# Performance work log

Measured on AMD Instinct MI355X. Metric: run time of the kernel, lower is better.

The kernel has to match this reference:

```python
import jax, jax.numpy as jnp
import numpy as np

H = 8          # attention heads
EPS = 1e-5     # LayerNorm eps (torch default)
B, T, E = 8, 1024, 128
D, DI, N, DC, R = 512, 1024, 16, 4, 32   # d_model, d_inner, d_state, d_conv, dt_rank
NT, NM = 6, 8                            # transformer layers, mamba layers
FF = 2048                                # transformer dim_feedforward (torch default)


def setup_inputs():
    key = jax.random.key(0)
    ks = iter(jax.random.split(key, 48))
    def rn(shape, scale=0.05):
        return jax.random.normal(next(ks), shape, jnp.float32) * scale
    return {
        "emb":      jax.random.normal(next(ks), (B, T, E), jnp.float32),
        # TransformerEncoder (6 post-norm layers), params stacked on leading layer dim
        "t_wqkv":   rn((NT, 3 * E, E)), "t_bqkv": jnp.zeros((NT, 3 * E), jnp.float32),
        "t_wo":     rn((NT, E, E)),     "t_bo":   jnp.zeros((NT, E), jnp.float32),
        "t_ln1w":   jnp.ones((NT, E), jnp.float32),  "t_ln1b": jnp.zeros((NT, E), jnp.float32),
        "t_w1":     rn((NT, FF, E)),    "t_b1":   jnp.zeros((NT, FF), jnp.float32),
        "t_w2":     rn((NT, E, FF)),    "t_b2":   jnp.zeros((NT, E), jnp.float32),
        "t_ln2w":   jnp.ones((NT, E), jnp.float32),  "t_ln2b": jnp.zeros((NT, E), jnp.float32),
        # Linear(emb_dim -> d_model)
        "w_in":     rn((D, E)), "b_in": jnp.zeros((D,), jnp.float32),
        # MambaBlocks (8 raw Mamba layers, no residual/norm), stacked
        "m_inproj": rn((NM, 2 * DI, D)),
        "m_convw":  rn((NM, DI, DC), 0.2), "m_convb": jnp.zeros((NM, DI), jnp.float32),
        "m_xproj":  rn((NM, R + 2 * N, DI)),
        "m_dtw":    rn((NM, DI, R), 0.1),
        "m_dtb":    jax.random.uniform(next(ks), (NM, DI), jnp.float32, -6.0, -3.0),
        "m_Alog":   jnp.log(jnp.tile(jnp.arange(1, N + 1, dtype=jnp.float32), (NM, DI, 1))),
        "m_D":      jnp.ones((NM, DI), jnp.float32),
        "m_outproj": rn((NM, D, DI)),
        # Linear(d_model -> emb_dim)
        "w_out":    rn((E, D)), "b_out": jnp.zeros((E,), jnp.float32),
    }


def _ln(x, w, b):
    mu = jnp.mean(x, -1, keepdims=True)
    var = jnp.var(x, -1, keepdims=True)
    return (x - mu) * jax.lax.rsqrt(var + EPS) * w + b


def _tlayer(x, p):
    wqkv, bqkv, wo, bo, ln1w, ln1b, w1, b1, w2, b2, ln2w, ln2b = p
    qkv = x @ wqkv.T + bqkv                        # (B,T,3E)
    q, k, v = jnp.split(qkv, 3, axis=-1)
    def heads(t):                                  # (B,T,E) -> (B,H,T,E//H)
        return t.reshape(B, T, H, E // H).transpose(0, 2, 1, 3)
    q, k, v = heads(q), heads(k), heads(v)
    scores = jnp.einsum("bhqd,bhkd->bhqk", q, k) / jnp.sqrt(jnp.float32(E // H))
    attn = jax.nn.softmax(scores, axis=-1)
    o = jnp.einsum("bhqk,bhkd->bhqd", attn, v).transpose(0, 2, 1, 3).reshape(B, T, E)
    x = _ln(x + o @ wo.T + bo, ln1w, ln1b)         # post-norm (torch default)
    ff = jax.nn.relu(x @ w1.T + b1) @ w2.T + b2
    return _ln(x + ff, ln2w, ln2b)


def _mamba_layer(x, p):
    inproj, convw, convb, xproj, dtw, dtb, Alog, Dp, outproj = p
    xz = x @ inproj.T                              # (B,T,2*DI)
    xi, z = jnp.split(xz, 2, axis=-1)
    # causal depthwise conv1d, kernel DC, left-padded
    xp = jnp.pad(xi, ((0, 0), (DC - 1, 0), (0, 0)))
    conv = sum(xp[:, k:k + T, :] * convw[:, k] for k in range(DC)) + convb
    xi = jax.nn.silu(conv)
    dbc = xi @ xproj.T                             # (B,T,R+2N)
    dt_r, Bt, Ct = dbc[..., :R], dbc[..., R:R + N], dbc[..., R + N:]
    dt = jax.nn.softplus(dt_r @ dtw.T + dtb)       # (B,T,DI)
    A = -jnp.exp(Alog)                             # (DI,N)
    def step(h, inputs):
        dt_t, B_t, C_t, x_t = inputs               # (B,DI),(B,N),(B,N),(B,DI)
        dA = jnp.exp(dt_t[:, :, None] * A)         # (B,DI,N)
        h = h * dA + (dt_t * x_t)[:, :, None] * B_t[:, None, :]
        y = jnp.einsum("bdn,bn->bd", h, C_t)
        return h, y
    h0 = jnp.zeros((B, DI, N), x.dtype)
    seq = (dt.transpose(1, 0, 2), Bt.transpose(1, 0, 2),
           Ct.transpose(1, 0, 2), xi.transpose(1, 0, 2))
    _, ys = jax.lax.scan(step, h0, seq)            # ys: (T,B,DI)
    y = ys.transpose(1, 0, 2) + Dp * xi
    y = y * jax.nn.silu(z)
    return y @ outproj.T                           # (B,T,D)


def reference(emb, t_wqkv, t_bqkv, t_wo, t_bo, t_ln1w, t_ln1b, t_w1, t_b1, t_w2, t_b2,
              t_ln2w, t_ln2b, w_in, b_in, m_inproj, m_convw, m_convb, m_xproj, m_dtw,
              m_dtb, m_Alog, m_D, m_outproj, w_out, b_out):
    x = emb
    tparams = (t_wqkv, t_bqkv, t_wo, t_bo, t_ln1w, t_ln1b, t_w1, t_b1, t_w2, t_b2, t_ln2w, t_ln2b)
    for i in range(NT):
        x = _tlayer(x, tuple(p[i] for p in tparams))
    x = x @ w_in.T + b_in                          # (B,T,D)
    mparams = (m_inproj, m_convw, m_convb, m_xproj, m_dtw, m_dtb, m_Alog, m_D, m_outproj)
    for i in range(NM):
        x = _mamba_layer(x, tuple(p[i] for p in mparams))
    return x @ w_out.T + b_out                     # (B,T,E)
```

## Files before the change

kernel.cpp:

```cpp
#include <hip/hip_runtime.h>
#include <math.h>

#define HB 8
#define TT 1024
#define NSTATE 16
#define NTT 6
#define NMM 8
#define MM (HB*TT)
#define EPSV 1e-5f
#define CHUNK 64
#define NCH (TT/CHUNK)
#define LSTR 72
#define AKS 128
#define VSTR 132

typedef _Float16 f16x8 __attribute__((ext_vector_type(8)));
typedef _Float16 f16x4 __attribute__((ext_vector_type(4)));
typedef float f32x4_t __attribute__((ext_vector_type(4)));

static __device__ inline void split8(const float4 a, const float4 b,
                                     f16x8& h, f16x8& l)
{
  float x[8] = {a.x, a.y, a.z, a.w, b.x, b.y, b.z, b.w};
#pragma unroll
  for (int i = 0; i < 8; i++) {
    _Float16 hi = (_Float16)x[i];
    h[i] = hi;
    l[i] = (_Float16)(x[i] - (float)hi);
  }
}

__global__ __launch_bounds__(256) void split_k(
    const float* __restrict__ X, _Float16* __restrict__ Hi,
    _Float16* __restrict__ Lo)
{
  const size_t i = ((size_t)blockIdx.x * 256 + threadIdx.x) * 4;
  float4 v = *(const float4*)&X[i];
  float x[4] = {v.x, v.y, v.z, v.w};
  f16x4 h, l;
#pragma unroll
  for (int j = 0; j < 4; j++) {
    _Float16 hi = (_Float16)x[j];
    h[j] = hi;
    l[j] = (_Float16)(x[j] - (float)hi);
  }
  *(f16x4*)&Hi[i] = h;
  *(f16x4*)&Lo[i] = l;
}

template<int TN>
__global__ __launch_bounds__(256) void gemm_mfma_t(
    const float* __restrict__ A, int lda,
    const float* __restrict__ W,
    const _Float16* __restrict__ Ahi, const _Float16* __restrict__ Alo,
    const _Float16* __restrict__ Whi, const _Float16* __restrict__ Wlo,
    const float* __restrict__ bias,
    float* __restrict__ C,
    float* __restrict__ P,
    int N, int K, int S, int act)
{
  __shared__ _Float16 As[128 * LSTR];
  __shared__ _Float16 Bs[TN * LSTR];
  const int tid = threadIdx.x;
  const int m0 = blockIdx.y * 128;
  const int n0 = blockIdx.x * TN;
  const int z = blockIdx.z;
  const int kchunk = K / S;
  const int kb = z * kchunk;
  const int ke = kb + kchunk;

  const int lr = tid >> 1;
  const int lh = tid & 1;
  const int lane = tid & 63;
  const int w = tid >> 6;
  const int quad = lane >> 4;
  const int l16 = lane & 15;

  const float* Arow = A + (size_t)(m0 + lr) * lda + lh * 16;
  const _Float16* AHrow = Ahi ? (Ahi + (size_t)(m0 + lr) * lda + lh * 16) : nullptr;
  const _Float16* ALrow = Ahi ? (Alo + (size_t)(m0 + lr) * lda + lh * 16) : nullptr;
  _Float16* Adst = &As[lr * LSTR + lh * 16];

  constexpr int MI = (TN == 128) ? 4 : 2;
  const int w0 = (TN == 128) ? (w & 1) : w;
  const int w1 = (TN == 128) ? (w >> 1) : 0;
  const int rowbase = (TN == 128) ? w0 * 64 : w0 * 32;

  f32x4_t acc[MI][4];
#pragma unroll
  for (int i = 0; i < MI; i++)
#pragma unroll
    for (int j = 0; j < 4; j++)
#pragma unroll
      for (int r = 0; r < 4; r++) acc[i][j][r] = 0.f;

  const _Float16* ab = &As[(rowbase + l16) * LSTR + quad * 8];
  const _Float16* bb = &Bs[(w1 * 64 + l16) * LSTR + quad * 8];

  const float* Wrow;
  const _Float16* WHrow = nullptr;
  const _Float16* WLrow = nullptr;
  _Float16* Bdst;
  if (TN == 128) {
    Wrow = W + (size_t)(n0 + lr) * K + lh * 16;
    if (Whi) {
      WHrow = Whi + (size_t)(n0 + lr) * K + lh * 16;
      WLrow = Wlo + (size_t)(n0 + lr) * K + lh * 16;
    }
    Bdst = &Bs[lr * LSTR + lh * 16];
  } else {
    const int br = tid >> 2;
    const int bo = (tid & 3) * 8;
    Wrow = W + (size_t)(n0 + br) * K + bo;
    if (Whi) {
      WHrow = Whi + (size_t)(n0 + br) * K + bo;
      WLrow = Wlo + (size_t)(n0 + br) * K + bo;
    }
    Bdst = &Bs[br * LSTR + bo];
  }

  for (int k0 = kb; k0 < ke; k0 += 32) {
    f16x8 ah0, ah1, al0, al1;
    float4 a0, a1, a2, a3;
    if (Ahi) {
      ah0 = *(const f16x8*)&AHrow[k0];
      ah1 = *(const f16x8*)&AHrow[k0 + 8];
      al0 = *(const f16x8*)&ALrow[k0];
      al1 = *(const f16x8*)&ALrow[k0 + 8];
    } else {
      a0 = *(const float4*)&Arow[k0];
      a1 = *(const float4*)&Arow[k0 + 4];
      a2 = *(const float4*)&Arow[k0 + 8];
      a3 = *(const float4*)&Arow[k0 + 12];
    }
    f16x8 wh0, wh1, wl0, wl1;
    float4 b0, b1, b2, b3;
    if (Whi) {
      wh0 = *(const f16x8*)&WHrow[k0];
      wl0 = *(const f16x8*)&WLrow[k0];
      if (TN == 128) {
        wh1 = *(const f16x8*)&WHrow[k0 + 8];
        wl1 = *(const f16x8*)&WLrow[k0 + 8];
      }
    } else {
      b0 = *(const float4*)&Wrow[k0];
      b1 = *(const float4*)&Wrow[k0 + 4];
      if (TN == 128) {
        b2 = *(const float4*)&Wrow[k0 + 8];
        b3 = *(const float4*)&Wrow[k0 + 12];
      }
    }
    __syncthreads();
    if (Ahi) {
      *(f16x8*)&Adst[0] = ah0; *(f16x8*)&Adst[8] = ah1;
      *(f16x8*)&Adst[32] = al0; *(f16x8*)&Adst[40] = al1;
    } else {
      f16x8 h, l;
      split8(a0, a1, h, l);
      *(f16x8*)&Adst[0] = h; *(f16x8*)&Adst[32] = l;
      split8(a2, a3, h, l);
      *(f16x8*)&Adst[8] = h; *(f16x8*)&Adst[40] = l;
    }
    if (Whi) {
      *(f16x8*)&Bdst[0] = wh0; *(f16x8*)&Bdst[32] = wl0;
      if (TN == 128) { *(f16x8*)&Bdst[8] = wh1; *(f16x8*)&Bdst[40] = wl1; }
    } else {
      f16x8 h, l;
      split8(b0, b1, h, l);
      *(f16x8*)&Bdst[0] = h; *(f16x8*)&Bdst[32] = l;
      if (TN == 128) {
        split8(b2, b3, h, l);
        *(f16x8*)&Bdst[8] = h; *(f16x8*)&Bdst[40] = l;
      }
    }
    __syncthreads();

    f16x8 bh[4], bl[4];
#pragma unroll
    for (int ni = 0; ni < 4; ni++) {
      bh[ni] = *(const f16x8*)&bb[ni * 16 * LSTR];
      bl[ni] = *(const f16x8*)&bb[ni * 16 * LSTR + 32];
    }
#pragma unroll
    for (int mi = 0; mi < MI; mi++) {
      f16x8 fah = *(const f16x8*)&ab[mi * 16 * LSTR];
      f16x8 fal = *(const f16x8*)&ab[mi * 16 * LSTR + 32];
#pragma unroll
      for (int ni = 0; ni < 4; ni++) {
        acc[mi][ni] = __builtin_amdgcn_mfma_f32_16x16x32_f16(fah, bh[ni], acc[mi][ni], 0, 0, 0);
        acc[mi][ni] = __builtin_amdgcn_mfma_f32_16x16x32_f16(fah, bl[ni], acc[mi][ni], 0, 0, 0);
        acc[mi][ni] = __builtin_amdgcn_mfma_f32_16x16x32_f16(fal, bh[ni], acc[mi][ni], 0, 0, 0);
      }
    }
  }

  float* dst = (S == 1) ? C : (P + (size_t)z * MM * N);
#pragma unroll
  for (int ni = 0; ni < 4; ni++) {
    const int n = n0 + w1 * 64 + ni * 16 + l16;
    const float bv = (S == 1 && bias) ? bias[n] : 0.f;
#pragma unroll
    for (int mi = 0; mi < MI; mi++) {
      const int mbase = m0 + rowbase + mi * 16 + quad * 4;
#pragma unroll
      for (int r = 0; r < 4; r++) {
        float v = acc[mi][ni][r] + bv;
        if (S == 1) {
          if (act == 1) v = fmaxf(v, 0.f);
          else if (act == 2) v = fmaxf(v, 0.f) + log1pf(__expf(-fabsf(v)));
        }
        dst[(size_t)(mbase + r) * N + n] = v;
      }
    }
  }
}

__global__ __launch_bounds__(256) void reduce_k(
    const float* __restrict__ P, const float* __restrict__ bias,
    float* __restrict__ C, int nmask, int S, int act, int stride4)
{
  const int idx = blockIdx.x * 256 + threadIdx.x;
  float4 a = *(const float4*)&P[(size_t)idx * 4];
  for (int z = 1; z < S; z++) {
    float4 p = *(const float4*)&P[(size_t)(idx + z * (size_t)stride4) * 4];
    a.x += p.x; a.y += p.y; a.z += p.z; a.w += p.w;
  }
  if (bias) {
    float4 bv = *(const float4*)&bias[(idx * 4) & nmask];
    a.x += bv.x; a.y += bv.y; a.z += bv.z; a.w += bv.w;
  }
  if (act == 1) {
    a.x = fmaxf(a.x, 0.f); a.y = fmaxf(a.y, 0.f);
    a.z = fmaxf(a.z, 0.f); a.w = fmaxf(a.w, 0.f);
  } else if (act == 2) {
    a.x = fmaxf(a.x, 0.f) + log1pf(__expf(-fabsf(a.x)));
    a.y = fmaxf(a.y, 0.f) + log1pf(__expf(-fabsf(a.y)));
    a.z = fmaxf(a.z, 0.f) + log1pf(__expf(-fabsf(a.z)));
    a.w = fmaxf(a.w, 0.f) + log1pf(__expf(-fabsf(a.w)));
  }
  *(float4*)&C[(size_t)idx * 4] = a;
}

__global__ __launch_bounds__(256) void attn_mfma_k(
    const float* __restrict__ qkv, float* __restrict__ o)
{
  __shared__ _Float16 Khi[AKS * 16], Klo[AKS * 16];
  __shared__ _Float16 Vthi[16 * VSTR], Vtlo[16 * VSTR];
  __shared__ float Pscr[4][16 * 18];

  const int tid = threadIdx.x;
  const int lane = tid & 63;
  const int wv = tid >> 6;
  const int quad = lane >> 4;
  const int l16 = lane & 15;
  const int qh = quad & 1;
  const int bh = blockIdx.y;
  const int b = bh >> 3;
  const int h = bh & 7;
  const int qb0 = blockIdx.x * 128;

  f16x8 qa[2];
#pragma unroll
  for (int u = 0; u < 2; u++) {
    const int qrow = qb0 + wv * 32 + u * 16 + l16;
    const float* qp = qkv + (size_t)(b * TT + qrow) * 384 + h * 16 + qh * 8;
    float4 x0 = *(const float4*)&qp[0];
    float4 x1 = *(const float4*)&qp[4];
    float xv[8] = {x0.x, x0.y, x0.z, x0.w, x1.x, x1.y, x1.z, x1.w};
#pragma unroll
    for (int j = 0; j < 8; j++) {
      float q = xv[j] * 0.25f;
      _Float16 hi = (_Float16)q;
      _Float16 lo = (_Float16)(q - (float)hi);
      qa[u][j] = (quad < 2) ? hi : lo;
    }
  }

  f32x4_t oacc[2];
  float lacc[2][4];
#pragma unroll
  for (int u = 0; u < 2; u++)
#pragma unroll
    for (int r = 0; r < 4; r++) { oacc[u][r] = 0.f; lacc[u][r] = 0.f; }

  float* Pw = &Pscr[wv][0];

  for (int ks = 0; ks < TT; ks += AKS) {
    __syncthreads();
    {
      const int key = tid >> 1, hf = tid & 1;
      const float* kp = qkv + (size_t)(b * TT + ks + key) * 384 + 128 + h * 16 + hf * 8;
      float4 k0 = *(const float4*)&kp[0];
      float4 k1 = *(const float4*)&kp[4];
      f16x8 vh, vl;
      split8(k0, k1, vh, vl);
      *(f16x8*)&Khi[key * 16 + hf * 8] = vh;
      *(f16x8*)&Klo[key * 16 + hf * 8] = vl;
      const float* vp = kp + 128;
      float4 v0 = *(const float4*)&vp[0];
      float4 v1 = *(const float4*)&vp[4];
      float vvv[8] = {v0.x, v0.y, v0.z, v0.w, v1.x, v1.y, v1.z, v1.w};
#pragma unroll
      for (int j = 0; j < 8; j++) {
        const int d = hf * 8 + j;
        _Float16 hi = (_Float16)vvv[j];
        Vthi[d * VSTR + key] = hi;
        Vtlo[d * VSTR + key] = (_Float16)(vvv[j] - (float)hi);
      }
    }
    __syncthreads();

    for (int kt = 0; kt < AKS; kt += 16) {
      f16x8 kfh = *(const f16x8*)&Khi[(kt + l16) * 16 + qh * 8];
      f16x8 kfl = *(const f16x8*)&Klo[(kt + l16) * 16 + qh * 8];
      const int vo = l16 * VSTR + kt + qh * 8;
      f16x4 va0 = *(const f16x4*)&Vthi[vo];
      f16x4 va1 = *(const f16x4*)&Vthi[vo + 4];
      f16x4 vb0 = *(const f16x4*)&Vtlo[vo];
      f16x4 vb1 = *(const f16x4*)&Vtlo[vo + 4];
      f16x8 vfh, vfl;
#pragma unroll
      for (int i = 0; i < 4; i++) {
        vfh[i] = va0[i]; vfh[4 + i] = va1[i];
        vfl[i] = vb0[i]; vfl[4 + i] = vb1[i];
      }

#pragma unroll
      for (int u = 0; u < 2; u++) {
        f32x4_t s;
#pragma unroll
        for (int r = 0; r < 4; r++) s[r] = 0.f;
        s = __builtin_amdgcn_mfma_f32_16x16x32_f16(qa[u], kfh, s, 0, 0, 0);
        s = __builtin_amdgcn_mfma_f32_16x16x32_f16(qa[u], kfl, s, 0, 0, 0);
        float p[4];
#pragma unroll
        for (int r = 0; r < 4; r++) {
          p[r] = __expf(s[r]);
          lacc[u][r] += p[r];
        }
        float* ps = Pw + (quad * 4) * 18 + l16;
        ps[0] = p[0]; ps[18] = p[1]; ps[36] = p[2]; ps[54] = p[3];
        __asm__ volatile("s_waitcnt lgkmcnt(0)" ::: "memory");
        const float* pr = Pw + l16 * 18 + qh * 8;
        f16x8 pa;
#pragma unroll
        for (int j = 0; j < 8; j++) {
          float pv = pr[j];
          _Float16 hi = (_Float16)pv;
          _Float16 lo = (_Float16)(pv - (float)hi);
          pa[j] = (quad < 2) ? hi : lo;
        }
        oacc[u] = __builtin_amdgcn_mfma_f32_16x16x32_f16(pa, vfh, oacc[u], 0, 0, 0);
        oacc[u] = __builtin_amdgcn_mfma_f32_16x16x32_f16(pa, vfl, oacc[u], 0, 0, 0);
        __asm__ volatile("s_waitcnt lgkmcnt(0)" ::: "memory");
      }
    }
  }

#pragma unroll
  for (int u = 0; u < 2; u++) {
#pragma unroll
    for (int r = 0; r < 4; r++) {
      float lv = lacc[u][r];
      lv += __shfl_xor(lv, 1);
      lv += __shfl_xor(lv, 2);
      lv += __shfl_xor(lv, 4);
      lv += __shfl_xor(lv, 8);
      const float inv = 1.f / lv;
      const int qrow = qb0 + wv * 32 + u * 16 + quad * 4 + r;
      o[(size_t)(b * TT + qrow) * 128 + h * 16 + l16] = oacc[u][r] * inv;
    }
  }
}

__global__ __launch_bounds__(256) void add_ln_k(
    const float* __restrict__ a, const float* __restrict__ bvec,
    const float* __restrict__ w, const float* __restrict__ bb,
    float* __restrict__ out)
{
  const int tid = threadIdx.x;
  const int wave = tid >> 6, lane = tid & 63;
  const size_t row = (size_t)blockIdx.x * 4 + wave;
  const float* pa = a + row * 128;
  const float* pb = bvec + row * 128;
  float v0 = pa[lane] + pb[lane];
  float v1 = pa[lane + 64] + pb[lane + 64];
  float s1 = v0 + v1, s2 = v0 * v0 + v1 * v1;
#pragma unroll
  for (int off = 32; off; off >>= 1) {
    s1 += __shfl_down(s1, off);
    s2 += __shfl_down(s2, off);
  }
  s1 = __shfl(s1, 0); s2 = __shfl(s2, 0);
  const float mean = s1 * (1.f / 128.f);
  const float var = s2 * (1.f / 128.f) - mean * mean;
  const float rs = rsqrtf(var + EPSV);
  out[row * 128 + lane]      = (v0 - mean) * rs * w[lane] + bb[lane];
  out[row * 128 + lane + 64] = (v1 - mean) * rs * w[lane + 64] + bb[lane + 64];
}

__global__ __launch_bounds__(256) void conv_silu_k(
    const float* __restrict__ xz, const float* __restrict__ cw,
    const float* __restrict__ cb, float* __restrict__ out)
{
  const int idx = blockIdx.x * 256 + threadIdx.x;
  const int di = idx & 1023;
  const int m = idx >> 10;
  const int t = m & (TT - 1);
  float acc = cb[di];
#pragma unroll
  for (int k = 0; k < 4; k++) {
    int tt = t + k - 3;
    if (tt >= 0) acc += xz[(size_t)(m + k - 3) * 2048 + di] * cw[di * 4 + k];
  }
  out[(size_t)m * 1024 + di] = acc / (1.f + __expf(-acc));
}

__global__ __launch_bounds__(64) void scan_partial_k(
    const float* __restrict__ dt,
    const float* __restrict__ dbc,
    const float* __restrict__ xi,
    const float* __restrict__ Alog,
    float* __restrict__ Pb, float* __restrict__ Sb)
{
  const int slice = blockIdx.x & 15;
  const int c = blockIdx.x >> 4;
  const int b = blockIdx.y;
  const int di = slice * 64 + threadIdx.x;

  float A[NSTATE];
#pragma unroll
  for (int n = 0; n < NSTATE; n++) A[n] = -__expf(Alog[di * NSTATE + n]);
  float h[NSTATE], P[NSTATE];
#pragma unroll
  for (int n = 0; n < NSTATE; n++) { h[n] = 0.f; P[n] = 1.f; }

  const size_t m0 = (size_t)b * TT + (size_t)c * CHUNK;
  for (int t = 0; t < CHUNK; t++) {
    const size_t m = m0 + t;
    const float dtv = dt[m * 1024 + di];
    const float xv  = xi[m * 1024 + di];
    const float dtx = dtv * xv;
#pragma unroll
    for (int n = 0; n < NSTATE; n++) {
      const float Bv = dbc[m * 64 + 32 + n];
      const float dA = __expf(dtv * A[n]);
      h[n] = h[n] * dA + dtx * Bv;
      P[n] *= dA;
    }
  }
  const size_t base = (((size_t)b * NCH + c) * NSTATE) * 1024 + di;
#pragma unroll
  for (int n = 0; n < NSTATE; n++) {
    Pb[base + (size_t)n * 1024] = P[n];
    Sb[base + (size_t)n * 1024] = h[n];
  }
}

__global__ __launch_bounds__(256) void scan_fix_k(
    float* __restrict__ Pb, const float* __restrict__ Sb)
{
  const int idx = blockIdx.x * 256 + threadIdx.x;
  const int b = idx >> 10;
  const int di = idx & 1023;
  float h[NSTATE];
#pragma unroll
  for (int n = 0; n < NSTATE; n++) h[n] = 0.f;
  for (int c = 0; c < NCH; c++) {
    const size_t base = (((size_t)b * NCH + c) * NSTATE) * 1024 + di;
    float P[NSTATE], S[NSTATE];
#pragma unroll
    for (int n = 0; n < NSTATE; n++) {
      P[n] = Pb[base + (size_t)n * 1024];
      S[n] = Sb[base + (size_t)n * 1024];
    }
#pragma unroll
    for (int n = 0; n < NSTATE; n++) {
      Pb[base + (size_t)n * 1024] = h[n];
      h[n] = P[n] * h[n] + S[n];
    }
  }
}

__global__ __launch_bounds__(64) void scan_final_k(
    const float* __restrict__ dt,
    const float* __restrict__ dbc,
    const float* __restrict__ xi,
    const float* __restrict__ xz,
    const float* __restrict__ Alog,
    const float* __restrict__ Dp,
    const float* __restrict__ Hin,
    float* __restrict__ Y)
{
  const int slice = blockIdx.x & 15;
  const int c = blockIdx.x >> 4;
  const int b = blockIdx.y;
  const int di = slice * 64 + threadIdx.x;

  float A[NSTATE];
#pragma unroll
  for (int n = 0; n < NSTATE; n++) A[n] = -__expf(Alog[di * NSTATE + n]);
  const float Dv = Dp[di];
  float h[NSTATE];
  const size_t hbase = (((size_t)b * NCH + c) * NSTATE) * 1024 + di;
#pragma unroll
  for (int n = 0; n < NSTATE; n++) h[n] = Hin[hbase + (size_t)n * 1024];

  const size_t m0 = (size_t)b * TT + (size_t)c * CHUNK;
  for (int t = 0; t < CHUNK; t++) {
    const size_t m = m0 + t;
    const float dtv = dt[m * 1024 + di];
    const float xv  = xi[m * 1024 + di];
    const float zv  = xz[m * 2048 + 1024 + di];
    const float dtx = dtv * xv;
    float y = 0.f;
#pragma unroll
    for (int n = 0; n < NSTATE; n++) {
      const float Bv = dbc[m * 64 + 32 + n];
      const float Cv = dbc[m * 64 + 48 + n];
      const float dA = __expf(dtv * A[n]);
      h[n] = h[n] * dA + dtx * Bv;
      y += h[n] * Cv;
    }
    y += Dv * xv;
    y *= zv / (1.f + __expf(-zv));
    Y[m * 1024 + di] = y;
  }
}

extern "C" void kernel_launch(void* const* d_in, const int* in_sizes, int n_in,
                              void* d_out, int out_size, void* d_ws, size_t ws_size,
                              hipStream_t stream)
{
  const float* emb      = (const float*)d_in[0];
  const float* t_wqkv   = (const float*)d_in[1];
  const float* t_bqkv   = (const float*)d_in[2];
  const float* t_wo     = (const float*)d_in[3];
  const float* t_bo     = (const float*)d_in[4];
  const float* t_ln1w   = (const float*)d_in[5];
  const float* t_ln1b   = (const float*)d_in[6];
  const float* t_w1     = (const float*)d_in[7];
  const float* t_b1     = (const float*)d_in[8];
  const float* t_w2     = (const float*)d_in[9];
  const float* t_b2     = (const float*)d_in[10];
  const float* t_ln2w   = (const float*)d_in[11];
  const float* t_ln2b   = (const float*)d_in[12];
  const float* w_in     = (const float*)d_in[13];
  const float* b_in     = (const float*)d_in[14];
  const float* m_inproj = (const float*)d_in[15];
  const float* m_convw  = (const float*)d_in[16];
  const float* m_convb  = (const float*)d_in[17];
  const float* m_xproj  = (const float*)d_in[18];
  const float* m_dtw    = (const float*)d_in[19];
  const float* m_dtb    = (const float*)d_in[20];
  const float* m_Alog   = (const float*)d_in[21];
  const float* m_D      = (const float*)d_in[22];
  const float* m_outproj= (const float*)d_in[23];
  const float* w_out    = (const float*)d_in[24];
  const float* b_out    = (const float*)d_in[25];

  float* ws = (float*)d_ws;
  float* X0   = ws;
  float* X1   = X0 + (size_t)MM * 512;
  float* Abuf = X1 + (size_t)MM * 512;
  float* Bf   = Abuf + (size_t)MM * 2048;
  float* Cf   = Bf + (size_t)MM * 1024;
  float* Yb   = Cf + (size_t)MM * 1024;
  float* Db   = Yb + (size_t)MM * 1024;

  const size_t baseFloats = (size_t)MM * 6208;
  const size_t wqE = (size_t)NTT * 384 * 128;
  const size_t woE = (size_t)NTT * 128 * 128;
  const size_t w1E = (size_t)NTT * 2048 * 128;
  const size_t w2E = (size_t)NTT * 128 * 2048;
  const size_t wiE = (size_t)512 * 128;
  const size_t ipE = (size_t)NMM * 2048 * 512;
  const size_t xpE = (size_t)NMM * 64 * 1024;
  const size_t dwE = (size_t)NMM * 1024 * 32;
  const size_t opE = (size_t)NMM * 512 * 1024;
  const size_t woutE = (size_t)128 * 512;
  const size_t totalWE = wqE + woE + w1E + w2E + wiE + ipE + xpE + dwE + opE + woutE;
  const bool pre = ws_size >= baseFloats * 4 + totalWE * 4;
  _Float16* Wa = (_Float16*)(ws + baseFloats);
  size_t off = 0;
  auto plane = [&](size_t cnt) { _Float16* p = Wa + off; off += 2 * cnt; return p; };
  _Float16* wqP = plane(wqE); _Float16* woP = plane(woE);
  _Float16* w1P = plane(w1E); _Float16* w2P = plane(w2E);
  _Float16* wiP = plane(wiE); _Float16* ipP = plane(ipE);
  _Float16* xpP = plane(xpE); _Float16* dwP = plane(dwE);
  _Float16* opP = plane(opE); _Float16* woutP = plane(woutE);

  dim3 blk(256);
  auto dosplit = [&](const float* src, _Float16* hi, size_t cnt) {
    hipLaunchKernelGGL(split_k, dim3((unsigned)(cnt / 1024)), blk, 0, stream,
                       src, hi, hi + cnt);
  };
  if (pre) {
    dosplit(t_wqkv, wqP, wqE);   dosplit(t_wo, woP, woE);
    dosplit(t_w1, w1P, w1E);     dosplit(t_w2, w2P, w2E);
    dosplit(w_in, wiP, wiE);     dosplit(m_inproj, ipP, ipE);
    dosplit(m_xproj, xpP, xpE);  dosplit(m_dtw, dwP, dwE);
    dosplit(m_outproj, opP, opE); dosplit(w_out, woutP, woutE);
  }

  auto gemm = [&](const float* A, int lda, const float* W, const float* bias,
                  float* C, int N, int K, int act, int S, float* P, bool tn64,
                  const _Float16* Ahi, const _Float16* Whi, size_t wcnt) {
    dim3 g(N / (tn64 ? 64 : 128), MM / 128, S);
    const _Float16* Alo = Ahi ? Ahi + (size_t)MM * K : nullptr;
    const _Float16* Wlo = (pre && Whi) ? Whi + wcnt : nullptr;
    const _Float16* Whi2 = pre ? Whi : nullptr;
    if (tn64)
      hipLaunchKernelGGL(gemm_mfma_t<64>, g, blk, 0, stream,
                         A, lda, W, Ahi, Alo, Whi2, Wlo,
                         S == 1 ? bias : nullptr, C, P, N, K, S, act);
    else
      hipLaunchKernelGGL(gemm_mfma_t<128>, g, blk, 0, stream,
                         A, lda, W, Ahi, Alo, Whi2, Wlo,
                         S == 1 ? bias : nullptr, C, P, N, K, S, act);
    if (S > 1) {
      int stride4 = (MM * N) / 4;
      hipLaunchKernelGGL(reduce_k, dim3(stride4 / 256), blk, 0, stream,
                         P, bias, C, N - 1, S, act, stride4);
    }
  };

  const float* x = emb;
  for (int l = 0; l < NTT; l++) {
    _Float16* aP = (_Float16*)Cf;
    hipLaunchKernelGGL(split_k, dim3(MM * 128 / 1024), blk, 0, stream,
                       x, aP, aP + (size_t)MM * 128);
    gemm(x, 128, t_wqkv + (size_t)l * 384 * 128, t_bqkv + l * 384,
         Abuf, 384, 128, 0, 1, nullptr, false,
         aP, wqP + (size_t)l * 384 * 128, wqE);
    hipLaunchKernelGGL(attn_mfma_k, dim3(TT / 128, HB * 8), blk, 0, stream,
                       Abuf, Yb);
    gemm(Yb, 128, t_wo + (size_t)l * 128 * 128, t_bo + l * 128,
         Cf, 128, 128, 0, 2, X1, true,
         nullptr, woP + (size_t)l * 128 * 128, woE);
    hipLaunchKernelGGL(add_ln_k, dim3(MM / 4), blk, 0, stream,
                       x, Cf, t_ln1w + l * 128, t_ln1b + l * 128, X0);
    aP = (_Float16*)Yb;
    hipLaunchKernelGGL(split_k, dim3(MM * 128 / 1024), blk, 0, stream,
                       X0, aP, aP + (size_t)MM * 128);
    gemm(X0, 128, t_w1 + (size_t)l * 2048 * 128, t_b1 + l * 2048,
         Abuf, 2048, 128, 1, 1, nullptr, false,
         aP, w1P + (size_t)l * 2048 * 128, w1E);
    gemm(Abuf, 2048, t_w2 + (size_t)l * 128 * 2048, t_b2 + l * 128,
         Cf, 128, 2048, 0, 8, Yb, false,
         nullptr, w2P + (size_t)l * 128 * 2048, w2E);
    hipLaunchKernelGGL(add_ln_k, dim3(MM / 4), blk, 0, stream,
                       X0, Cf, t_ln2w + l * 128, t_ln2b + l * 128, X0);
    x = X0;
  }

  {
    _Float16* aP = (_Float16*)Cf;
    hipLaunchKernelGGL(split_k, dim3(MM * 128 / 1024), blk, 0, stream,
                       X0, aP, aP + (size_t)MM * 128);
    gemm(X0, 128, w_in, b_in, X1, 512, 128, 0, 1, nullptr, false,
         aP, wiP, wiE);
  }

  float* xc = X1;
  float* xo = X0;
  for (int l = 0; l < NMM; l++) {
    _Float16* aP = (_Float16*)Cf;
    hipLaunchKernelGGL(split_k, dim3(MM * 512 / 1024), blk, 0, stream,
                       xc, aP, aP + (size_t)MM * 512);
    gemm(xc, 512, m_inproj + (size_t)l * 2048 * 512, nullptr,
         Abuf, 2048, 512, 0, 1, nullptr, false,
         aP, ipP + (size_t)l * 2048 * 512, ipE);
    hipLaunchKernelGGL(conv_silu_k, dim3(MM * 1024 / 256), blk, 0, stream,
                       Abuf, m_convw + (size_t)l * 1024 * 4, m_convb + l * 1024, Bf);
    gemm(Bf, 1024, m_xproj + (size_t)l * 64 * 1024, nullptr,
         Db, 64, 1024, 0, 4, xo, true,
         nullptr, xpP + (size_t)l * 64 * 1024, xpE);
    gemm(Db, 64, m_dtw + (size_t)l * 1024 * 32, m_dtb + l * 1024,
         Cf, 1024, 32, 2, 1, nullptr, false,
         nullptr, dwP + (size_t)l * 1024 * 32, dwE);

    float* Pb = xo;
    float* Sb = xo + (size_t)HB * NCH * NSTATE * 1024;
    hipLaunchKernelGGL(scan_partial_k, dim3(16 * NCH, HB), dim3(64), 0, stream,
                       Cf, Db, Bf, m_Alog + (size_t)l * 1024 * 16, Pb, Sb);
    hipLaunchKernelGGL(scan_fix_k, dim3(MM / 1024 * 4), blk, 0, stream, Pb, Sb);
    hipLaunchKernelGGL(scan_final_k, dim3(16 * NCH, HB), dim3(64), 0, stream,
                       Cf, Db, Bf, Abuf,
                       m_Alog + (size_t)l * 1024 * 16, m_D + l * 1024, Pb, Yb);

    gemm(Yb, 1024, m_outproj + (size_t)l * 512 * 1024, nullptr,
         xo, 512, 1024, 0, 2, Abuf, false,
         nullptr, opP + (size_t)l * 512 * 1024, opE);
    float* tmp = xc; xc = xo; xo = tmp;
  }

  gemm(xc, 512, w_out, b_out, (float*)d_out, 128, 512, 0, 4, Yb, false,
       nullptr, woutP, woutE);
}
```

Measured before the change: 3.783 ms.

## Prefetch next K-tile into registers and use fragment-ordered LDS layout in MFMA GEMM

The GEMM kernel now issues the global loads for the next 32-wide K slice right after the shared-memory store barrier, so the loads overlap with the MFMA work on the current slice. Shared memory is reorganised into a fragment-major layout (row block, hi/lo, quad, row, 8 halves), which makes the stores contiguous per thread and makes the MFMA operand reads linear. This is meant to hide global-memory latency and reduce LDS bank conflicts. The cost is higher register pressure from holding the prefetched tiles, and the global access pattern changes to 16-byte chunks spread across rows.

```diff
diff --git a/kernel.cpp b/kernel.cpp
--- a/kernel.cpp
+++ b/kernel.cpp
@@ -10,7 +10,6 @@
 #define EPSV 1e-5f
 #define CHUNK 64
 #define NCH (TT/CHUNK)
-#define LSTR 72
 #define AKS 128
 #define VSTR 132
 
@@ -59,8 +58,10 @@
     float* __restrict__ P,
     int N, int K, int S, int act)
 {
-  __shared__ _Float16 As[128 * LSTR];
-  __shared__ _Float16 Bs[TN * LSTR];
+  constexpr int BCH = (TN == 128) ? 1024 : 512;
+  __shared__ _Float16 As[1024 * 8];
+  __shared__ _Float16 Bs[BCH * 8];
+
   const int tid = threadIdx.x;
   const int m0 = blockIdx.y * 128;
   const int n0 = blockIdx.x * TN;
@@ -69,22 +70,20 @@
   const int kb = z * kchunk;
   const int ke = kb + kchunk;
 
-  const int lr = tid >> 1;
-  const int lh = tid & 1;
   const int lane = tid & 63;
   const int w = tid >> 6;
   const int quad = lane >> 4;
   const int l16 = lane & 15;
 
-  const float* Arow = A + (size_t)(m0 + lr) * lda + lh * 16;
-  const _Float16* AHrow = Ahi ? (Ahi + (size_t)(m0 + lr) * lda + lh * 16) : nullptr;
-  const _Float16* ALrow = Ahi ? (Alo + (size_t)(m0 + lr) * lda + lh * 16) : nullptr;
-  _Float16* Adst = &As[lr * LSTR + lh * 16];
-
   constexpr int MI = (TN == 128) ? 4 : 2;
   const int w0 = (TN == 128) ? (w & 1) : w;
   const int w1 = (TN == 128) ? (w >> 1) : 0;
   const int rowbase = (TN == 128) ? w0 * 64 : w0 * 32;
+  const int rbA0 = (TN == 128) ? w0 * 4 : w * 2;
+  const int cb0 = w1 * 4;
+
+  const bool preA = (Ahi != nullptr);
+  const bool preB = (Whi != nullptr);
 
   f32x4_t acc[MI][4];
 #pragma unroll
@@ -94,97 +93,105 @@
 #pragma unroll
       for (int r = 0; r < 4; r++) acc[i][j][r] = 0.f;
 
-  const _Float16* ab = &As[(rowbase + l16) * LSTR + quad * 8];
-  const _Float16* bb = &Bs[(w1 * 64 + l16) * LSTR + quad * 8];
-
-  const float* Wrow;
-  const _Float16* WHrow = nullptr;
-  const _Float16* WLrow = nullptr;
-  _Float16* Bdst;
-  if (TN == 128) {
-    Wrow = W + (size_t)(n0 + lr) * K + lh * 16;
-    if (Whi) {
-      WHrow = Whi + (size_t)(n0 + lr) * K + lh * 16;
-      WLrow = Wlo + (size_t)(n0 + lr) * K + lh * 16;
-    }
-    Bdst = &Bs[lr * LSTR + lh * 16];
-  } else {
-    const int br = tid >> 2;
-    const int bo = (tid & 3) * 8;
-    Wrow = W + (size_t)(n0 + br) * K + bo;
-    if (Whi) {
-      WHrow = Whi + (size_t)(n0 + br) * K + bo;
-      WLrow = Wlo + (size_t)(n0 + br) * K + bo;
-    }
-    Bdst = &Bs[br * LSTR + bo];
-  }
-
+  f16x8 ra[4], rb[4];
+  float4 fa[4], fb[4];
+
+  auto loadA = [&](int k0) {
+    if (preA) {
+#pragma unroll
+      for (int i = 0; i < 4; i++) {
+        const int c = tid + 256 * i;
+        const int r = c & 15, qd = (c >> 4) & 3, hl = (c >> 6) & 1, rbk = c >> 7;
+        const _Float16* src = (hl ? Alo : Ahi)
+            + (size_t)(m0 + rbk * 16 + r) * lda + k0 + qd * 8;
+        ra[i] = *(const f16x8*)src;
+      }
+    } else {
+#pragma unroll
+      for (int i = 0; i < 2; i++) {
+        const int g = tid + 256 * i;
+        const int r = g & 15, qd = (g >> 4) & 3, rbk = g >> 6;
+        const float* src = A + (size_t)(m0 + rbk * 16 + r) * lda + k0 + qd * 8;
+        fa[2 * i] = *(const float4*)src;
+        fa[2 * i + 1] = *(const float4*)(src + 4);
+      }
+    }
+  };
+  auto loadB = [&](int k0) {
+    if (preB) {
+#pragma unroll
+      for (int i = 0; i < BCH / 256; i++) {
+        const int c = tid + 256 * i;
+        const int r = c & 15, qd = (c >> 4) & 3, hl = (c >> 6) & 1, cb = c >> 7;
+        const _Float16* src = (hl ? Wlo : Whi)
+            + (size_t)(n0 + cb * 16 + r) * K + k0 + qd * 8;
+        rb[i] = *(const f16x8*)src;
+      }
+    } else {
+#pragma unroll
+      for (int i = 0; i < ((TN == 128) ? 2 : 1); i++) {
+        const int g = tid + 256 * i;
+        const int r = g & 15, qd = (g >> 4) & 3, cb = g >> 6;
+        const float* src = W + (size_t)(n0 + cb * 16 + r) * K + k0 + qd * 8;
+        fb[2 * i] = *(const float4*)src;
+        fb[2 * i + 1] = *(const float4*)(src + 4);
+      }
+    }
+  };
+  auto storeA = [&]() {
+    if (preA) {
+#pragma unroll
+      for (int i = 0; i < 4; i++)
+        *(f16x8*)&As[(tid + 256 * i) * 8] = ra[i];
+    } else {
+#pragma unroll
+      for (int i = 0; i < 2; i++) {
+        const int g = tid + 256 * i;
+        const int r = g & 15, qd = (g >> 4) & 3, rbk = g >> 6;
+        f16x8 h, l;
+        split8(fa[2 * i], fa[2 * i + 1], h, l);
+        *(f16x8*)&As[(((rbk * 2 + 0) * 4 + qd) * 16 + r) * 8] = h;
+        *(f16x8*)&As[(((rbk * 2 + 1) * 4 + qd) * 16 + r) * 8] = l;
+      }
+    }
+  };
+  auto storeB = [&]() {
+    if (preB) {
+#pragma unroll
+      for (int i = 0; i < BCH / 256; i++)
+        *(f16x8*)&Bs[(tid + 256 * i) * 8] = rb[i];
+    } else {
+#pragma unroll
+      for (int i = 0; i < ((TN == 128) ? 2 : 1); i++) {
+        const int g = tid + 256 * i;
+        const int r = g & 15, qd = (g >> 4) & 3, cb = g >> 6;
+        f16x8 h, l;
+        split8(fb[2 * i], fb[2 * i + 1], h, l);
+        *(f16x8*)&Bs[(((cb * 2 + 0) * 4 + qd) * 16 + r) * 8] = h;
+        *(f16x8*)&Bs[(((cb * 2 + 1) * 4 + qd) * 16 + r) * 8] = l;
+      }
+    }
+  };
+
+  loadA(kb); loadB(kb);
   for (int k0 = kb; k0 < ke; k0 += 32) {
-    f16x8 ah0, ah1, al0, al1;
-    float4 a0, a1, a2, a3;
-    if (Ahi) {
-      ah0 = *(const f16x8*)&AHrow[k0];
-      ah1 = *(const f16x8*)&AHrow[k0 + 8];
-      al0 = *(const f16x8*)&ALrow[k0];
-      al1 = *(const f16x8*)&ALrow[k0 + 8];
-    } else {
-      a0 = *(const float4*)&Arow[k0];
-      a1 = *(const float4*)&Arow[k0 + 4];
-      a2 = *(const float4*)&Arow[k0 + 8];
-      a3 = *(const float4*)&Arow[k0 + 12];
-    }
-    f16x8 wh0, wh1, wl0, wl1;
-    float4 b0, b1, b2, b3;
-    if (Whi) {
-      wh0 = *(const f16x8*)&WHrow[k0];
-      wl0 = *(const f16x8*)&WLrow[k0];
-      if (TN == 128) {
-        wh1 = *(const f16x8*)&WHrow[k0 + 8];
-        wl1 = *(const f16x8*)&WLrow[k0 + 8];
-      }
-    } else {
-      b0 = *(const float4*)&Wrow[k0];
-      b1 = *(const float4*)&Wrow[k0 + 4];
-      if (TN == 128) {
-        b2 = *(const float4*)&Wrow[k0 + 8];
-        b3 = *(const float4*)&Wrow[k0 + 12];
-      }
-    }
     __syncthreads();
-    if (Ahi) {
-      *(f16x8*)&Adst[0] = ah0; *(f16x8*)&Adst[8] = ah1;
-      *(f16x8*)&Adst[32] = al0; *(f16x8*)&Adst[40] = al1;
-    } else {
-      f16x8 h, l;
-      split8(a0, a1, h, l);
-      *(f16x8*)&Adst[0] = h; *(f16x8*)&Adst[32] = l;
-      split8(a2, a3, h, l);
-      *(f16x8*)&Adst[8] = h; *(f16x8*)&Adst[40] = l;
-    }
-    if (Whi) {
-      *(f16x8*)&Bdst[0] = wh0; *(f16x8*)&Bdst[32] = wl0;
-      if (TN == 128) { *(f16x8*)&Bdst[8] = wh1; *(f16x8*)&Bdst[40] = wl1; }
-    } else {
-      f16x8 h, l;
-      split8(b0, b1, h, l);
-      *(f16x8*)&Bdst[0] = h; *(f16x8*)&Bdst[32] = l;
-      if (TN == 128) {
-        split8(b2, b3, h, l);
-        *(f16x8*)&Bdst[8] = h; *(f16x8*)&Bdst[40] = l;
-      }
-    }
+    storeA(); storeB();
     __syncthreads();
+    if (k0 + 32 < ke) { loadA(k0 + 32); loadB(k0 + 32); }
 
     f16x8 bh[4], bl[4];
 #pragma unroll
     for (int ni = 0; ni < 4; ni++) {
-      bh[ni] = *(const f16x8*)&bb[ni * 16 * LSTR];
-      bl[ni] = *(const f16x8*)&bb[ni * 16 * LSTR + 32];
+      const int cb = cb0 + ni;
+      bh[ni] = *(const f16x8*)&Bs[(((cb * 2 + 0) * 4 + quad) * 16 + l16) * 8];
+      bl[ni] = *(const f16x8*)&Bs[(((cb * 2 + 1) * 4 + quad) * 16 + l16) * 8];
     }
 #pragma unroll
     for (int mi = 0; mi < MI; mi++) {
-      f16x8 fah = *(const f16x8*)&ab[mi * 16 * LSTR];
-      f16x8 fal = *(const f16x8*)&ab[mi * 16 * LSTR + 32];
+      const int rbk = rbA0 + mi;
+      f16x8 fah = *(const f16x8*)&As[(((rbk * 2 + 0) * 4 + quad) * 16 + l16) * 8];
+      f16x8 fal = *(const f16x8*)&As[(((rbk * 2 + 1) * 4 + quad) * 16 + l16) * 8];
 #pragma unroll
       for (int ni = 0; ni < 4; ni++) {
         acc[mi][ni] = __builtin_amdgcn_mfma_f32_16x16x32_f16(fah, bh[ni], acc[mi][ni], 0, 0, 0);
```

After: 4.264 ms. +12.7%, slower.
